# Optimization experiments

Hardware: AMD Instinct MI355X
Metric: run time of the kernel (lower is better)

Reference implementation:

```python
import jax, jax.numpy as jnp
import numpy as np

B, L, D, H, HD, K, MAXLEN = 4, 2048, 1024, 16, 64, 32, 2048


def setup_inputs() -> dict:
    key = jax.random.key(0)
    ks = jax.random.split(key, 8)
    s = 0.02  # init scale (stand-in for lecun-normal magnitude)
    return {
        "inputs_q": jax.random.normal(ks[0], (B, L, D), jnp.float32),
        "inputs_kv": jax.random.normal(ks[1], (B, L, D), jnp.float32),
        "Wv": jax.random.normal(ks[2], (D, H, HD), jnp.float32) * s,   # value DenseGeneral kernel
        "bv": jnp.zeros((H, HD), jnp.float32),                          # value bias
        "r1": jax.random.normal(ks[3], (H, MAXLEN, K), jnp.float32) * s,  # param 'random1'
        "r2": jax.random.normal(ks[4], (H, K, MAXLEN), jnp.float32) * s,  # param 'random2'
        "Wo": jax.random.normal(ks[5], (H, HD, D), jnp.float32) * s,   # output DenseGeneral kernel
        "bo": jnp.zeros((D,), jnp.float32),                             # output bias
    }


def reference(inputs_q, inputs_kv, Wv, bv, r1, r2, Wo, bo):
    # SynthesizerAttention with ignore_dot_product=True, mode='factorized_random',
    # no masks, deterministic (no dropout).
    qlen = inputs_q.shape[-2]
    kvlen = inputs_kv.shape[-2]
    # value projection: [B, Lkv, H, HD]; key=value, query=inputs_q (unused for scores)
    v = jnp.einsum('bnd,dhk->bnhk', inputs_kv, Wv) + bv
    # factorized random synthetic scores: [H, Lq, Lkv]
    syn = jnp.einsum('hlk,hkn->hln', r1[:, :qlen, :], r2[:, :, :kvlen])
    # softmax over the key/value axis (norm_dims in synthetic_attention).
    # Scores are batch-independent, so softmax once per head (broadcast over B).
    attn = jax.nn.softmax(syn, axis=-1)
    # weighted sum over values: [B, Lq, H, HD]
    y = jnp.einsum('hln,bnhk->blhk', attn, v)
    # output projection over (H, HD): [B, Lq, D]
    return jnp.einsum('blhk,hkd->bld', y, Wo) + bo
```

## Files before the change

kernel.cpp:

```cpp
#include <hip/hip_runtime.h>
#include <hip/hip_bf16.h>

#define LL 2048

typedef __bf16 bf16x8 __attribute__((ext_vector_type(8)));
typedef __bf16 bf16x4 __attribute__((ext_vector_type(4)));
typedef float f32x4 __attribute__((ext_vector_type(4)));

__device__ inline void gl_lds16(const __bf16* g, __bf16* l) {
    __builtin_amdgcn_global_load_lds((const __attribute__((address_space(1))) void*)g,
                                     (__attribute__((address_space(3))) void*)l, 16, 0, 0);
}

__global__ __launch_bounds__(256) void prep(const float* __restrict__ inputs_kv,
                                            const float* __restrict__ r1,
                                            const float* __restrict__ Wv,
                                            const float* __restrict__ Wo,
                                            const float* __restrict__ r2,
                                            __bf16* __restrict__ A1,
                                            __bf16* __restrict__ r1b,
                                            __bf16* __restrict__ Wvt,
                                            __bf16* __restrict__ Wot,
                                            __bf16* __restrict__ r2t) {
    __shared__ float Ls[32][65];
    int bid = blockIdx.x;
    const int tid = threadIdx.x;
    if (bid < 4608) {
        const float* in = (bid < 4096) ? inputs_kv : r1;
        __bf16* out = (bid < 4096) ? A1 : r1b;
        const int t = ((bid < 4096) ? bid : bid - 4096) * 256 + tid;
        const float4* in4 = (const float4*)in;
        float4 f0 = in4[t * 2], f1 = in4[t * 2 + 1];
        bf16x8 o;
        o[0] = (__bf16)f0.x; o[1] = (__bf16)f0.y; o[2] = (__bf16)f0.z; o[3] = (__bf16)f0.w;
        o[4] = (__bf16)f1.x; o[5] = (__bf16)f1.y; o[6] = (__bf16)f1.z; o[7] = (__bf16)f1.w;
        *(bf16x8*)&out[(size_t)t * 8] = o;
        return;
    }
    bid -= 4608;
    const float* in;
    __bf16* out;
    int R, C, r0, c0;
    if (bid < 512) {
        in = Wv; out = Wvt; R = 1024; C = 1024;
        c0 = (bid & 15) * 64; r0 = (bid >> 4) * 32;
    } else if (bid < 1024) {
        bid -= 512;
        in = Wo; out = Wot; R = 1024; C = 1024;
        c0 = (bid & 15) * 64; r0 = (bid >> 4) * 32;
    } else {
        bid -= 1024;
        const int bz = bid >> 5;
        in = r2 + (size_t)bz * 65536; out = r2t + (size_t)bz * 65536;
        R = 32; C = 2048;
        c0 = (bid & 31) * 64; r0 = 0;
    }
#pragma unroll
    for (int p = 0; p < 2; ++p) {
        int f = tid + 256 * p;
        int row = f >> 4, c4 = (f & 15) << 2;
        float4 v = *(const float4*)&in[(size_t)(r0 + row) * C + c0 + c4];
        Ls[row][c4 + 0] = v.x; Ls[row][c4 + 1] = v.y;
        Ls[row][c4 + 2] = v.z; Ls[row][c4 + 3] = v.w;
    }
    __syncthreads();
    const int orow = tid >> 2, rc = (tid & 3) << 3;
    bf16x8 o;
#pragma unroll
    for (int j = 0; j < 8; ++j) o[j] = (__bf16)Ls[rc + j][orow];
    *(bf16x8*)&out[(size_t)(c0 + orow) * R + r0 + rc] = o;
}

template <int MODE>
__global__ __launch_bounds__(256) void gemm_bt(const __bf16* __restrict__ A,
                                               const __bf16* __restrict__ Bt,
                                               const float* __restrict__ bias,
                                               void* __restrict__ Cout,
                                               int M, int N, int K) {
    __shared__ alignas(16) __bf16 As[128 * 32];
    __shared__ alignas(16) __bf16 Bs[128 * 32];
    const int tid = threadIdx.x;
    const int lane = tid & 63;
    const int wid = __builtin_amdgcn_readfirstlane(tid >> 6);
    const int f = blockIdx.y * 8 + blockIdx.x;
    const int g = (f & 7) * 64 + (f >> 3);
    const int row0 = (g >> 3) * 128, col0 = (g & 7) * 128;
    const int l15 = lane & 15, quad = lane >> 4;
    const int wr = wid & 1, wc = wid >> 1;
    const int s0 = wid * 2, s1 = s0 + 1;

    const __bf16* ga0 = A + (size_t)(row0 + s0 * 16 + (lane >> 2)) * K + ((lane & 3) << 3);
    const __bf16* ga1 = ga0 + (size_t)16 * K;
    const __bf16* gb0 = Bt + (size_t)(col0 + s0 * 16 + (lane >> 2)) * K + ((lane & 3) << 3);
    const __bf16* gb1 = gb0 + (size_t)16 * K;
    __bf16* la0 = As + s0 * 512;
    __bf16* la1 = As + s1 * 512;
    __bf16* lb0 = Bs + s0 * 512;
    __bf16* lb1 = Bs + s1 * 512;

    f32x4 acc[4][4];
#pragma unroll
    for (int i = 0; i < 4; ++i)
#pragma unroll
        for (int j = 0; j < 4; ++j) acc[i][j] = (f32x4){0.f, 0.f, 0.f, 0.f};

    for (int k0 = 0; k0 < K; k0 += 32) {
        __syncthreads();
        gl_lds16(ga0 + k0, la0);
        gl_lds16(ga1 + k0, la1);
        gl_lds16(gb0 + k0, lb0);
        gl_lds16(gb1 + k0, lb1);
        __syncthreads();
        bf16x8 af[4], bfv[4];
#pragma unroll
        for (int i = 0; i < 4; ++i)
            af[i] = *(const bf16x8*)&As[(wr * 64 + i * 16 + l15) * 32 + quad * 8];
#pragma unroll
        for (int j = 0; j < 4; ++j)
            bfv[j] = *(const bf16x8*)&Bs[(wc * 64 + j * 16 + l15) * 32 + quad * 8];
#pragma unroll
        for (int i = 0; i < 4; ++i)
#pragma unroll
            for (int j = 0; j < 4; ++j)
                acc[i][j] = __builtin_amdgcn_mfma_f32_16x16x32_bf16(af[i], bfv[j], acc[i][j], 0, 0, 0);
    }

#pragma unroll
    for (int i = 0; i < 4; ++i) {
        const int rg = row0 + wr * 64 + i * 16 + quad * 4;
#pragma unroll
        for (int j = 0; j < 4; ++j) {
            const int cg = col0 + wc * 64 + j * 16 + l15;
            const float bb = bias[cg];
            if (MODE == 0) {
                const int b = rg >> 11, n = rg & 2047;
                const int h = cg >> 6, hd = cg & 63;
                const int nc = n >> 6, ks = (n >> 5) & 1, qj = (n >> 3) & 3, j0 = n & 7;
                const int jt = hd >> 4, fl = hd & 15;
                __bf16* V3 = (__bf16*)Cout;
                bf16x4 v;
#pragma unroll
                for (int r = 0; r < 4; ++r) v[r] = (__bf16)(acc[i][j][r] + bb);
                *(bf16x4*)&V3[(size_t)(((h * 32 + nc) * 4 + b) * 4096) +
                              (jt * 2 + ks) * 512 + fl * 32 + qj * 8 + j0] = v;
            } else {
                float* Cf = (float*)Cout;
#pragma unroll
                for (int r = 0; r < 4; ++r)
                    Cf[(size_t)(rg + r) * N + cg] = acc[i][j][r] + bb;
            }
        }
    }
}

__global__ __launch_bounds__(512) void attn_pv_v7(const __bf16* __restrict__ r1b,
                                                  const __bf16* __restrict__ r2t,
                                                  const __bf16* __restrict__ V3,
                                                  __bf16* __restrict__ yb) {
    __shared__ alignas(16) __bf16 Ps[2 * 2 * 4 * 1024];
    const int tid = threadIdx.x;
    const int lane = tid & 63;
    const int w = __builtin_amdgcn_readfirstlane(tid >> 6);
    const int b = w & 3, lh = w >> 2;
    const int l15 = lane & 15, quad = lane >> 4;
    const int id = blockIdx.x;
    const int h = id & 15;
    const int l0 = (id >> 4) << 7;

    bf16x8 bf1[4];
#pragma unroll
    for (int i = 0; i < 4; ++i)
        bf1[i] = *(const bf16x8*)&r1b[(size_t)(h * 2048 + l0 + lh * 64 + i * 16 + l15) * 32 + quad * 8];

    const __bf16* r2p = r2t + (size_t)(h * 2048 + b * 16 + l15) * 32 + quad * 8;
    const __bf16* vp = V3 + (size_t)((h * 32) * 4 + b) * 4096 + l15 * 32 + quad * 8;

    bf16x8 r2f = *(const bf16x8*)r2p;
    bf16x8 vpf[4][2];
#pragma unroll
    for (int jt = 0; jt < 4; ++jt)
#pragma unroll
        for (int ks = 0; ks < 2; ++ks)
            vpf[jt][ks] = *(const bf16x8*)(vp + (jt * 2 + ks) * 512);

    bf16x8 ones;
#pragma unroll
    for (int e = 0; e < 8; ++e) ones[e] = (__bf16)1.0f;

    f32x4 acc[4][4];
    f32x4 den[4];
#pragma unroll
    for (int i = 0; i < 4; ++i) {
        den[i] = (f32x4){0.f, 0.f, 0.f, 0.f};
#pragma unroll
        for (int j = 0; j < 4; ++j) acc[i][j] = (f32x4){0.f, 0.f, 0.f, 0.f};
    }
    const f32x4 zero4 = {0.f, 0.f, 0.f, 0.f};

    const int kw = b >> 1;
    const int jg = (b & 1) * 2 + (quad >> 1);
    const int q4 = (quad & 1) * 4;
    const int swz = (l15 >> 1) & 3;

    f32x4 s[4];
#pragma unroll
    for (int i = 0; i < 4; ++i)
        s[i] = __builtin_amdgcn_mfma_f32_16x16x32_bf16(r2f, bf1[i], zero4, 0, 0, 0);
    r2f = *(const bf16x8*)(r2p + 2048);
    {
        __bf16* ps = &Ps[lh * 4096];
#pragma unroll
        for (int i = 0; i < 4; ++i) {
            bf16x4 p4;
#pragma unroll
            for (int r = 0; r < 4; ++r) p4[r] = (__bf16)__expf(s[i][r]);
            *(bf16x4*)&ps[i * 1024 + kw * 512 + l15 * 32 + ((jg ^ swz) << 3) + q4] = p4;
        }
    }

    for (int c = 0; c < 32; ++c) {
        asm volatile("s_waitcnt lgkmcnt(0)" ::: "memory");
        __builtin_amdgcn_s_barrier();
        const __bf16* ps_r = &Ps[((c & 1) * 2 + lh) * 4096];
        bf16x8 pa[4][2];
#pragma unroll
        for (int i = 0; i < 4; ++i)
#pragma unroll
            for (int ks = 0; ks < 2; ++ks)
                pa[i][ks] = *(const bf16x8*)&ps_r[i * 1024 + ks * 512 + l15 * 32 + ((quad ^ swz) << 3)];
#pragma unroll
        for (int i = 0; i < 4; ++i)
            s[i] = __builtin_amdgcn_mfma_f32_16x16x32_bf16(r2f, bf1[i], zero4, 0, 0, 0);
        const int i2 = (c < 30) ? (c + 2) : 31;
        r2f = *(const bf16x8*)(r2p + (size_t)i2 * 2048);
#pragma unroll
        for (int ks = 0; ks < 2; ++ks) {
#pragma unroll
            for (int i = 0; i < 4; ++i) {
#pragma unroll
                for (int jt = 0; jt < 4; ++jt)
                    acc[i][jt] = __builtin_amdgcn_mfma_f32_16x16x32_bf16(pa[i][ks], vpf[jt][ks],
                                                                         acc[i][jt], 0, 0, 0);
                den[i] = __builtin_amdgcn_mfma_f32_16x16x32_bf16(pa[i][ks], ones, den[i], 0, 0, 0);
            }
        }
        __bf16* ps_w = &Ps[(((c + 1) & 1) * 2 + lh) * 4096];
#pragma unroll
        for (int i = 0; i < 4; ++i) {
            bf16x4 p4;
#pragma unroll
            for (int r = 0; r < 4; ++r) p4[r] = (__bf16)__expf(s[i][r]);
            *(bf16x4*)&ps_w[i * 1024 + kw * 512 + l15 * 32 + ((jg ^ swz) << 3) + q4] = p4;
        }
        const int cv = (c < 31) ? 1 : 0;
        vp += cv * 16384;
#pragma unroll
        for (int jt = 0; jt < 4; ++jt)
#pragma unroll
            for (int ks = 0; ks < 2; ++ks)
                vpf[jt][ks] = *(const bf16x8*)(vp + (jt * 2 + ks) * 512);
    }

#pragma unroll
    for (int i = 0; i < 4; ++i) {
#pragma unroll
        for (int r = 0; r < 4; ++r) {
            const float iv = 1.0f / den[i][r];
            const int l = l0 + lh * 64 + i * 16 + quad * 4 + r;
            const size_t rowbase = ((size_t)b * LL + l) * 1024 + h * 64;
#pragma unroll
            for (int jt = 0; jt < 4; ++jt)
                yb[rowbase + jt * 16 + l15] = (__bf16)(acc[i][jt][r] * iv);
        }
    }
}

extern "C" void kernel_launch(void* const* d_in, const int* in_sizes, int n_in,
                              void* d_out, int out_size, void* d_ws, size_t ws_size,
                              hipStream_t stream) {
    const float* inputs_kv = (const float*)d_in[1];
    const float* Wv = (const float*)d_in[2];
    const float* bv = (const float*)d_in[3];
    const float* r1 = (const float*)d_in[4];
    const float* r2 = (const float*)d_in[5];
    const float* Wo = (const float*)d_in[6];
    const float* bo = (const float*)d_in[7];
    float* out = (float*)d_out;

    char* ws = (char*)d_ws;
    const size_t MB = 1024 * 1024;
    __bf16* A1  = (__bf16*)(ws);
    __bf16* Wvt = (__bf16*)(ws + 16 * MB);
    __bf16* Wot = (__bf16*)(ws + 18 * MB);
    __bf16* r1b = (__bf16*)(ws + 20 * MB);
    __bf16* r2t = (__bf16*)(ws + 22 * MB);
    __bf16* V3  = (__bf16*)(ws + 24 * MB);
    __bf16* yb  = (__bf16*)(ws + 40 * MB);

    prep<<<6144, 256, 0, stream>>>(inputs_kv, r1, Wv, Wo, r2, A1, r1b, Wvt, Wot, r2t);
    gemm_bt<0><<<dim3(8, 64), 256, 0, stream>>>(A1, Wvt, bv, V3, 8192, 1024, 1024);
    attn_pv_v7<<<256, 512, 0, stream>>>(r1b, r2t, V3, yb);
    gemm_bt<1><<<dim3(8, 64), 256, 0, stream>>>(yb, Wot, bo, out, 8192, 1024, 1024);
}
```

Measured before the change: 212.9 us.

## Double-buffer GEMM LDS tiles and halve attention rows per block

The GEMM main loop now stages tiles in two LDS buffers. The next K-tile's global-to-LDS loads are issued before computing on the current tile, which removes one barrier per iteration and overlaps loads with MFMA work. The attention kernel now handles 64 query rows per block instead of 128 and launches 512 blocks, with a 4-blocks-per-CU launch bound. That is meant to raise occupancy and spread work across more CUs, at the cost of loading each V chunk and r2 fragment twice as often per output row.

```diff
diff --git a/kernel.cpp b/kernel.cpp
--- a/kernel.cpp
+++ b/kernel.cpp
@@ -77,8 +77,8 @@
                                                const float* __restrict__ bias,
                                                void* __restrict__ Cout,
                                                int M, int N, int K) {
-    __shared__ alignas(16) __bf16 As[128 * 32];
-    __shared__ alignas(16) __bf16 Bs[128 * 32];
+    __shared__ alignas(16) __bf16 As[2][128 * 32];
+    __shared__ alignas(16) __bf16 Bs[2][128 * 32];
     const int tid = threadIdx.x;
     const int lane = tid & 63;
     const int wid = __builtin_amdgcn_readfirstlane(tid >> 6);
@@ -93,10 +93,6 @@
     const __bf16* ga1 = ga0 + (size_t)16 * K;
     const __bf16* gb0 = Bt + (size_t)(col0 + s0 * 16 + (lane >> 2)) * K + ((lane & 3) << 3);
     const __bf16* gb1 = gb0 + (size_t)16 * K;
-    __bf16* la0 = As + s0 * 512;
-    __bf16* la1 = As + s1 * 512;
-    __bf16* lb0 = Bs + s0 * 512;
-    __bf16* lb1 = Bs + s1 * 512;
 
     f32x4 acc[4][4];
 #pragma unroll
@@ -104,20 +100,31 @@
 #pragma unroll
         for (int j = 0; j < 4; ++j) acc[i][j] = (f32x4){0.f, 0.f, 0.f, 0.f};
 
-    for (int k0 = 0; k0 < K; k0 += 32) {
+    const int nt = K >> 5;
+    gl_lds16(ga0, As[0] + s0 * 512);
+    gl_lds16(ga1, As[0] + s1 * 512);
+    gl_lds16(gb0, Bs[0] + s0 * 512);
+    gl_lds16(gb1, Bs[0] + s1 * 512);
+
+    for (int t = 0; t < nt; ++t) {
         __syncthreads();
-        gl_lds16(ga0 + k0, la0);
-        gl_lds16(ga1 + k0, la1);
-        gl_lds16(gb0 + k0, lb0);
-        gl_lds16(gb1 + k0, lb1);
-        __syncthreads();
+        if (t + 1 < nt) {
+            const int k0 = (t + 1) << 5;
+            const int nb = (t + 1) & 1;
+            gl_lds16(ga0 + k0, As[nb] + s0 * 512);
+            gl_lds16(ga1 + k0, As[nb] + s1 * 512);
+            gl_lds16(gb0 + k0, Bs[nb] + s0 * 512);
+            gl_lds16(gb1 + k0, Bs[nb] + s1 * 512);
+        }
+        const __bf16* as = As[t & 1];
+        const __bf16* bs = Bs[t & 1];
         bf16x8 af[4], bfv[4];
 #pragma unroll
         for (int i = 0; i < 4; ++i)
-            af[i] = *(const bf16x8*)&As[(wr * 64 + i * 16 + l15) * 32 + quad * 8];
+            af[i] = *(const bf16x8*)&as[(wr * 64 + i * 16 + l15) * 32 + quad * 8];
 #pragma unroll
         for (int j = 0; j < 4; ++j)
-            bfv[j] = *(const bf16x8*)&Bs[(wc * 64 + j * 16 + l15) * 32 + quad * 8];
+            bfv[j] = *(const bf16x8*)&bs[(wc * 64 + j * 16 + l15) * 32 + quad * 8];
 #pragma unroll
         for (int i = 0; i < 4; ++i)
 #pragma unroll
@@ -153,11 +160,11 @@
     }
 }
 
-__global__ __launch_bounds__(512) void attn_pv_v7(const __bf16* __restrict__ r1b,
-                                                  const __bf16* __restrict__ r2t,
-                                                  const __bf16* __restrict__ V3,
-                                                  __bf16* __restrict__ yb) {
-    __shared__ alignas(16) __bf16 Ps[2 * 2 * 4 * 1024];
+__global__ __launch_bounds__(512, 4) void attn_pv_v8(const __bf16* __restrict__ r1b,
+                                                     const __bf16* __restrict__ r2t,
+                                                     const __bf16* __restrict__ V3,
+                                                     __bf16* __restrict__ yb) {
+    __shared__ alignas(16) __bf16 Ps[2 * 2 * 2 * 1024];
     const int tid = threadIdx.x;
     const int lane = tid & 63;
     const int w = __builtin_amdgcn_readfirstlane(tid >> 6);
@@ -165,12 +172,12 @@
     const int l15 = lane & 15, quad = lane >> 4;
     const int id = blockIdx.x;
     const int h = id & 15;
-    const int l0 = (id >> 4) << 7;
-
-    bf16x8 bf1[4];
-#pragma unroll
-    for (int i = 0; i < 4; ++i)
-        bf1[i] = *(const bf16x8*)&r1b[(size_t)(h * 2048 + l0 + lh * 64 + i * 16 + l15) * 32 + quad * 8];
+    const int l0 = (id >> 4) << 6;
+
+    bf16x8 bf1[2];
+#pragma unroll
+    for (int i = 0; i < 2; ++i)
+        bf1[i] = *(const bf16x8*)&r1b[(size_t)(h * 2048 + l0 + lh * 32 + i * 16 + l15) * 32 + quad * 8];
 
     const __bf16* r2p = r2t + (size_t)(h * 2048 + b * 16 + l15) * 32 + quad * 8;
     const __bf16* vp = V3 + (size_t)((h * 32) * 4 + b) * 4096 + l15 * 32 + quad * 8;
@@ -187,10 +194,10 @@
 #pragma unroll
     for (int e = 0; e < 8; ++e) ones[e] = (__bf16)1.0f;
 
-    f32x4 acc[4][4];
-    f32x4 den[4];
-#pragma unroll
-    for (int i = 0; i < 4; ++i) {
+    f32x4 acc[2][4];
+    f32x4 den[2];
+#pragma unroll
+    for (int i = 0; i < 2; ++i) {
         den[i] = (f32x4){0.f, 0.f, 0.f, 0.f};
 #pragma unroll
         for (int j = 0; j < 4; ++j) acc[i][j] = (f32x4){0.f, 0.f, 0.f, 0.f};
@@ -202,15 +209,15 @@
     const int q4 = (quad & 1) * 4;
     const int swz = (l15 >> 1) & 3;
 
-    f32x4 s[4];
-#pragma unroll
-    for (int i = 0; i < 4; ++i)
+    f32x4 s[2];
+#pragma unroll
+    for (int i = 0; i < 2; ++i)
         s[i] = __builtin_amdgcn_mfma_f32_16x16x32_bf16(r2f, bf1[i], zero4, 0, 0, 0);
     r2f = *(const bf16x8*)(r2p + 2048);
     {
-        __bf16* ps = &Ps[lh * 4096];
-#pragma unroll
-        for (int i = 0; i < 4; ++i) {
+        __bf16* ps = &Ps[lh * 2048];
+#pragma unroll
+        for (int i = 0; i < 2; ++i) {
             bf16x4 p4;
 #pragma unroll
             for (int r = 0; r < 4; ++r) p4[r] = (__bf16)__expf(s[i][r]);
@@ -221,22 +228,22 @@
     for (int c = 0; c < 32; ++c) {
         asm volatile("s_waitcnt lgkmcnt(0)" ::: "memory");
         __builtin_amdgcn_s_barrier();
-        const __bf16* ps_r = &Ps[((c & 1) * 2 + lh) * 4096];
-        bf16x8 pa[4][2];
-#pragma unroll
-        for (int i = 0; i < 4; ++i)
+        const __bf16* ps_r = &Ps[(c & 1) * 4096 + lh * 2048];
+        bf16x8 pa[2][2];
+#pragma unroll
+        for (int i = 0; i < 2; ++i)
 #pragma unroll
             for (int ks = 0; ks < 2; ++ks)
                 pa[i][ks] = *(const bf16x8*)&ps_r[i * 1024 + ks * 512 + l15 * 32 + ((quad ^ swz) << 3)];
 #pragma unroll
-        for (int i = 0; i < 4; ++i)
+        for (int i = 0; i < 2; ++i)
             s[i] = __builtin_amdgcn_mfma_f32_16x16x32_bf16(r2f, bf1[i], zero4, 0, 0, 0);
         const int i2 = (c < 30) ? (c + 2) : 31;
         r2f = *(const bf16x8*)(r2p + (size_t)i2 * 2048);
 #pragma unroll
         for (int ks = 0; ks < 2; ++ks) {
 #pragma unroll
-            for (int i = 0; i < 4; ++i) {
+            for (int i = 0; i < 2; ++i) {
 #pragma unroll
                 for (int jt = 0; jt < 4; ++jt)
                     acc[i][jt] = __builtin_amdgcn_mfma_f32_16x16x32_bf16(pa[i][ks], vpf[jt][ks],
@@ -244,9 +251,9 @@
                 den[i] = __builtin_amdgcn_mfma_f32_16x16x32_bf16(pa[i][ks], ones, den[i], 0, 0, 0);
             }
         }
-        __bf16* ps_w = &Ps[(((c + 1) & 1) * 2 + lh) * 4096];
-#pragma unroll
-        for (int i = 0; i < 4; ++i) {
+        __bf16* ps_w = &Ps[((c + 1) & 1) * 4096 + lh * 2048];
+#pragma unroll
+        for (int i = 0; i < 2; ++i) {
             bf16x4 p4;
 #pragma unroll
             for (int r = 0; r < 4; ++r) p4[r] = (__bf16)__expf(s[i][r]);
@@ -262,11 +269,11 @@
     }
 
 #pragma unroll
-    for (int i = 0; i < 4; ++i) {
+    for (int i = 0; i < 2; ++i) {
 #pragma unroll
         for (int r = 0; r < 4; ++r) {
             const float iv = 1.0f / den[i][r];
-            const int l = l0 + lh * 64 + i * 16 + quad * 4 + r;
+            const int l = l0 + lh * 32 + i * 16 + quad * 4 + r;
             const size_t rowbase = ((size_t)b * LL + l) * 1024 + h * 64;
 #pragma unroll
             for (int jt = 0; jt < 4; ++jt)
@@ -299,6 +306,6 @@
 
     prep<<<6144, 256, 0, stream>>>(inputs_kv, r1, Wv, Wo, r2, A1, r1b, Wvt, Wot, r2t);
     gemm_bt<0><<<dim3(8, 64), 256, 0, stream>>>(A1, Wvt, bv, V3, 8192, 1024, 1024);
-    attn_pv_v7<<<256, 512, 0, stream>>>(r1b, r2t, V3, yb);
+    attn_pv_v8<<<512, 512, 0, stream>>>(r1b, r2t, V3, yb);
     gemm_bt<1><<<dim3(8, 64), 256, 0, stream>>>(yb, Wot, bo, out, 8192, 1024, 1024);
 }
```

Result: slower. 237.7 us (+11.6%).

## Double-buffer A tile in LDS and load B fragments directly to registers

Applied to the files above, without the earlier changes.

The bf16 GEMM now double-buffers the A tile in LDS, prefetching the next k-slice while the current one is consumed, and drops one barrier per iteration. The B operand bypasses LDS and is loaded straight from global memory into register fragments, with a one-step register prefetch. This aims to overlap memory latency with MFMA work and cut LDS traffic. The cost is that each wave redundantly fetches its own B fragments from global memory (wr pairs duplicate loads) and register pressure goes up. There is also a possible race: only one barrier per iteration now guards the LDS buffer reuse, and the async LDS load completion wait relies on that barrier.

```diff
diff --git a/kernel.cpp b/kernel.cpp
--- a/kernel.cpp
+++ b/kernel.cpp
@@ -77,8 +77,7 @@
                                                const float* __restrict__ bias,
                                                void* __restrict__ Cout,
                                                int M, int N, int K) {
-    __shared__ alignas(16) __bf16 As[128 * 32];
-    __shared__ alignas(16) __bf16 Bs[128 * 32];
+    __shared__ alignas(16) __bf16 As[2][128 * 32];
     const int tid = threadIdx.x;
     const int lane = tid & 63;
     const int wid = __builtin_amdgcn_readfirstlane(tid >> 6);
@@ -91,12 +90,7 @@
 
     const __bf16* ga0 = A + (size_t)(row0 + s0 * 16 + (lane >> 2)) * K + ((lane & 3) << 3);
     const __bf16* ga1 = ga0 + (size_t)16 * K;
-    const __bf16* gb0 = Bt + (size_t)(col0 + s0 * 16 + (lane >> 2)) * K + ((lane & 3) << 3);
-    const __bf16* gb1 = gb0 + (size_t)16 * K;
-    __bf16* la0 = As + s0 * 512;
-    __bf16* la1 = As + s1 * 512;
-    __bf16* lb0 = Bs + s0 * 512;
-    __bf16* lb1 = Bs + s1 * 512;
+    const __bf16* gB = Bt + (size_t)(col0 + wc * 64 + l15) * K + quad * 8;
 
     f32x4 acc[4][4];
 #pragma unroll
@@ -104,25 +98,39 @@
 #pragma unroll
         for (int j = 0; j < 4; ++j) acc[i][j] = (f32x4){0.f, 0.f, 0.f, 0.f};
 
-    for (int k0 = 0; k0 < K; k0 += 32) {
+    const int nt = K >> 5;
+    gl_lds16(ga0, As[0] + s0 * 512);
+    gl_lds16(ga1, As[0] + s1 * 512);
+    bf16x8 bcur[4], bnxt[4];
+#pragma unroll
+    for (int j = 0; j < 4; ++j)
+        bcur[j] = *(const bf16x8*)(gB + (size_t)j * 16 * K);
+
+    for (int t = 0; t < nt; ++t) {
         __syncthreads();
-        gl_lds16(ga0 + k0, la0);
-        gl_lds16(ga1 + k0, la1);
-        gl_lds16(gb0 + k0, lb0);
-        gl_lds16(gb1 + k0, lb1);
-        __syncthreads();
-        bf16x8 af[4], bfv[4];
+        if (t + 1 < nt) {
+            const int k0 = (t + 1) << 5;
+            const int nb = (t + 1) & 1;
+            gl_lds16(ga0 + k0, As[nb] + s0 * 512);
+            gl_lds16(ga1 + k0, As[nb] + s1 * 512);
+#pragma unroll
+            for (int j = 0; j < 4; ++j)
+                bnxt[j] = *(const bf16x8*)(gB + (size_t)j * 16 * K + k0);
+        }
+        const __bf16* as = As[t & 1];
+        bf16x8 af[4];
 #pragma unroll
         for (int i = 0; i < 4; ++i)
-            af[i] = *(const bf16x8*)&As[(wr * 64 + i * 16 + l15) * 32 + quad * 8];
-#pragma unroll
-        for (int j = 0; j < 4; ++j)
-            bfv[j] = *(const bf16x8*)&Bs[(wc * 64 + j * 16 + l15) * 32 + quad * 8];
+            af[i] = *(const bf16x8*)&as[(wr * 64 + i * 16 + l15) * 32 + quad * 8];
 #pragma unroll
         for (int i = 0; i < 4; ++i)
 #pragma unroll
             for (int j = 0; j < 4; ++j)
-                acc[i][j] = __builtin_amdgcn_mfma_f32_16x16x32_bf16(af[i], bfv[j], acc[i][j], 0, 0, 0);
+                acc[i][j] = __builtin_amdgcn_mfma_f32_16x16x32_bf16(af[i], bcur[j], acc[i][j], 0, 0, 0);
+        if (t + 1 < nt) {
+#pragma unroll
+            for (int j = 0; j < 4; ++j) bcur[j] = bnxt[j];
+        }
     }
 
 #pragma unroll
```

After: 233.8 us. 9.8% more time.
